# Kernel optimization log

Measured on AMD Instinct MI355X. Metric: run time of the kernel, lower is better.

The kernel has to match this reference:

```python
import jax, jax.numpy as jnp
import numpy as np
from jax import lax

MAX_U = 5
MAX_V = 5
BN_EPS = 1e-5


def _conv(x, w, b, p):
    # NCHW conv with symmetric padding p (torch Conv2d padding=p)
    y = lax.conv_general_dilated(x, w, (1, 1), [(p, p), (p, p)],
                                 dimension_numbers=('NCHW', 'OIHW', 'NCHW'))
    return y + b[None, :, None, None]


def _branch(x, w3, b3, w5, b5, w7, b7):
    a3 = jax.nn.relu(_conv(x, w3, b3, 1))
    a5 = jax.nn.relu(_conv(jnp.concatenate([a3, x], 1), w5, b5, 2))
    a7 = jax.nn.relu(_conv(jnp.concatenate([a5, x], 1), w7, b7, 3))
    return jnp.concatenate([a3, a5, a7], 1)  # [B, 448, H, W]


def _dct_basis(n, kmax, dtype):
    # orthonormal DCT-II basis rows for frequencies u < kmax: [kmax, n]
    i = jnp.arange(n, dtype=dtype)
    u = jnp.arange(kmax, dtype=dtype)
    basis = jnp.cos(jnp.pi * (2.0 * i[None, :] + 1.0) * u[:, None] / (2.0 * n))
    scale = jnp.where(u == 0, jnp.sqrt(1.0 / n), jnp.sqrt(2.0 / n))
    return basis * scale[:, None]


def setup_inputs() -> dict:
    key = jax.random.key(0)
    ks = iter(jax.random.split(key, 64))

    def w(shape, s=0.05):
        return (jax.random.normal(next(ks), shape, jnp.float32) * s)

    cin = 3  # input_channels per group (x has 2*cin = 6 channels)
    inp = {"x": jax.random.normal(next(ks), (16, 6, 64, 64), jnp.float32)}
    for g in (1, 2):
        for b in (1, 2):
            inp[f"g{g}b{b}c3_w"] = w((64, cin, 3, 3))
            inp[f"g{g}b{b}c3_b"] = w((64,))
            inp[f"g{g}b{b}c5_w"] = w((128, 64 + cin, 5, 5))
            inp[f"g{g}b{b}c5_b"] = w((128,))
            inp[f"g{g}b{b}c7_w"] = w((256, 128 + cin, 7, 7))
            inp[f"g{g}b{b}c7_b"] = w((256,))
    inp["gap_w"] = w((12, 1792)); inp["gap_b"] = w((12,))
    inp["dct_w"] = w((12, 1792)); inp["dct_b"] = w((12,))
    inp["bn_gamma"] = jnp.ones((1792,), jnp.float32)
    inp["bn_beta"] = jnp.zeros((1792,), jnp.float32)
    inp["bn_mean"] = jnp.zeros((1792,), jnp.float32)
    inp["bn_var"] = jnp.ones((1792,), jnp.float32)
    return inp


def reference(x,
              g1b1c3_w, g1b1c3_b, g1b1c5_w, g1b1c5_b, g1b1c7_w, g1b1c7_b,
              g1b2c3_w, g1b2c3_b, g1b2c5_w, g1b2c5_b, g1b2c7_w, g1b2c7_b,
              g2b1c3_w, g2b1c3_b, g2b1c5_w, g2b1c5_b, g2b1c7_w, g2b1c7_b,
              g2b2c3_w, g2b2c3_b, g2b2c5_w, g2b2c5_b, g2b2c7_w, g2b2c7_b,
              gap_w, gap_b, dct_w, dct_b, bn_gamma, bn_beta, bn_mean, bn_var):
    B, C, H, W = x.shape  # C is even (6)
    half = C // 2
    x1, x2 = x[:, :half], x[:, half:]
    out1 = jnp.concatenate([
        _branch(x1, g1b1c3_w, g1b1c3_b, g1b1c5_w, g1b1c5_b, g1b1c7_w, g1b1c7_b),
        _branch(x1, g1b2c3_w, g1b2c3_b, g1b2c5_w, g1b2c5_b, g1b2c7_w, g1b2c7_b)], 1)
    out2 = jnp.concatenate([
        _branch(x2, g2b1c3_w, g2b1c3_b, g2b1c5_w, g2b1c5_b, g2b1c7_w, g2b1c7_b),
        _branch(x2, g2b2c3_w, g2b2c3_b, g2b2c5_w, g2b2c5_b, g2b2c7_w, g2b2c7_b)], 1)
    concat_out = jnp.concatenate([out1, out2], 1)  # [B, 1792, H, W]

    # GAP head
    gap = concat_out.mean((2, 3))  # [B, 1792]
    gap_pred = gap @ gap_w.T + gap_b

    # Batched multi-frequency DCT compression: low-frequency 5x5 block of the
    # 2D DCT-II of each channel, averaged -> one scalar per channel.
    Bh = _dct_basis(H, MAX_U, x.dtype)  # [5, H]
    Bw = _dct_basis(W, MAX_V, x.dtype)  # [5, W]
    coeff = jnp.einsum('bchw,uh,vw->bcuv', concat_out, Bh, Bw)  # [B,1792,5,5]
    dct_feat = coeff.mean((2, 3))  # [B, 1792]

    # BatchNorm1d (inference with running stats); dropout is identity in eval.
    bn = bn_gamma * (dct_feat - bn_mean) / jnp.sqrt(bn_var + BN_EPS) + bn_beta
    dct_pred = bn @ dct_w.T + dct_b
    return gap_pred, dct_pred
```

## Files before the change

kernel.cpp:

```cpp
#include <hip/hip_runtime.h>
#include <hip/hip_bf16.h>
#include <math.h>

#define HW 64
#define NPIX 4096
#define NB 16
#define NCH 1792

typedef __bf16 bf16;
typedef __bf16 bf16x8 __attribute__((ext_vector_type(8)));
typedef float f32x4 __attribute__((ext_vector_type(4)));

struct PtrQuad { const float* p[4]; };

constexpr size_t W3SZ = 9 * 1 * 64 * 32;
constexpr size_t W5SZ = 25 * 3 * 128 * 32;
constexpr size_t W7SZ = 49 * 5 * 256 * 32;
constexpr size_t WBR  = W3SZ + W5SZ + W7SZ;

__global__ __launch_bounds__(256) void init_kernel(float* __restrict__ gap_sum,
                                                   float* __restrict__ dct_sum,
                                                   float* __restrict__ dctw) {
    int tid = blockIdx.x * 256 + threadIdx.x;
    if (tid < NB * NCH) { gap_sum[tid] = 0.f; dct_sum[tid] = 0.f; }
    if (blockIdx.x == 0 && threadIdx.x < HW) {
        int i = threadIdx.x;
        float s = 0.f;
        for (int u = 0; u < 5; ++u) {
            float scale = (u == 0) ? 0.125f : 0.17677669529663687f;
            s += cosf(3.14159265358979323846f * (2.f * i + 1.f) * u / 128.f) * scale;
        }
        dctw[i] = s * 0.2f;
    }
}

__global__ __launch_bounds__(256) void prep_x_kernel(const float* __restrict__ x,
                                                     bf16* __restrict__ xpad) {
    int tid = blockIdx.x * 256 + threadIdx.x;
    if (tid >= NB * 2 * NPIX * 32) return;
    int c = tid & 31;
    int pix = (tid >> 5) & (NPIX - 1);
    int g = (tid >> 17) & 1;
    int b = tid >> 18;
    float v = (c < 3) ? x[((size_t)(b * 6 + g * 3 + c)) * NPIX + pix] : 0.f;
    xpad[tid] = (bf16)v;
}

template <int K, int CHUNKS, int CIN_ACT, int COUT>
__global__ __launch_bounds__(256) void prep_w_all(PtrQuad src, bf16* __restrict__ dst) {
    constexpr int CIN = CIN_ACT + 3;
    constexpr int TOT = K * K * CHUNKS * COUT * 32;
    int tid = blockIdx.x * 256 + threadIdx.x;
    if (tid >= 4 * TOT) return;
    int br = tid / TOT;
    int idx = tid - br * TOT;
    int cc = idx & 31;
    int co = (idx >> 5) % COUT;
    int rest = idx / (32 * COUT);
    int chunk = rest % CHUNKS;
    int ks = rest / CHUNKS;
    int ky = ks / K, kx = ks % K;
    int ci;
    if (chunk < CHUNKS - 1) ci = chunk * 32 + cc;
    else ci = (cc < 3) ? (CIN_ACT + cc) : -1;
    const float* w = src.p[br];
    float v = (ci >= 0) ? w[(((size_t)co * CIN + ci) * K + ky) * K + kx] : 0.f;
    dst[(size_t)br * WBR + idx] = (bf16)v;
}

template <int K, int CHUNKS, int COUT, int NBLK, bool STORE>
__global__ __launch_bounds__(256, 2) void conv_mfma(
    const bf16* __restrict__ act_in, size_t a_in_brs,
    const bf16* __restrict__ xpad,
    const bf16* __restrict__ wall, size_t stage_woff,
    PtrQuad biasq,
    bf16* __restrict__ act_out, size_t a_out_brs,
    float* __restrict__ gap_sum, float* __restrict__ dct_sum,
    int stage_coff, const float* __restrict__ dctw, int br0)
{
    constexpr int PAD = K / 2;
    constexpr int R = 4;
    constexpr int HR = R + K - 1;
    constexpr int WC = HW + K - 1;
    constexpr int ACT_CHUNKS = CHUNKS - 1;
    constexpr int AS = ACT_CHUNKS * 32;
    constexpr int WN = NBLK / 32;
    constexpr int NUNITS = 4 * HR * WC;
    constexpr int SEGU = HR * WC + 1;
    constexpr int CW = CHUNKS * COUT * 32;

    __shared__ __align__(16) bf16 s_in[4 * SEGU * 8];

    const int tid = threadIdx.x;
    const int lane = tid & 63;
    const int wv = tid >> 6;
    const int wm = wv >> 1;
    const int wn = wv & 1;
    const int q = lane >> 4;
    const int ln = lane & 15;

    const int bz = blockIdx.z;
    const int b = bz & 15;
    const int lbr = bz >> 4;
    const int br = br0 + lbr;
    const int g = br >> 1;

    const int row0 = blockIdx.x * R;
    const int n0g = blockIdx.y * NBLK + wn * (NBLK / 2);

    const bf16* wrep = wall + (size_t)br * WBR + stage_woff;
    const float* bias = biasq.p[br];

    int abase[8];
#pragma unroll
    for (int t = 0; t < 8; ++t) {
        int lr = wm * 2 + (t >> 2);
        int ct = (t & 3) * 16;
        abase[t] = (q * SEGU + lr * WC + ct + ln) * 8;
    }
    const int lane_w = ln * 32 + q * 8;

    f32x4 acc[8][WN];
#pragma unroll
    for (int t = 0; t < 8; ++t)
#pragma unroll
        for (int u = 0; u < WN; ++u) acc[t][u] = f32x4{0.f, 0.f, 0.f, 0.f};

    const bf16* xsrc = xpad + ((size_t)(b * 2 + g)) * NPIX * 32;
    const bf16* actb = act_in + lbr * a_in_brs + (size_t)b * NPIX * AS;

#pragma unroll 1
    for (int chunk = 0; chunk < CHUNKS; ++chunk) {
        __syncthreads();
        const bf16* src;
        int stride;
        if (chunk < ACT_CHUNKS) { src = actb + chunk * 32; stride = AS; }
        else                    { src = xsrc;              stride = 32; }
        for (int uidx = tid; uidx < NUNITS; uidx += 256) {
            int kseg = uidx / (HR * WC);
            int rem = uidx - kseg * (HR * WC);
            int rr = rem / WC;
            int col = rem - rr * WC;
            int gr = row0 + rr - PAD;
            int gc = col - PAD;
            bf16x8 v;
#pragma unroll
            for (int j = 0; j < 8; ++j) v[j] = (bf16)0.f;
            if (gr >= 0 && gr < HW && gc >= 0 && gc < HW)
                v = *(const bf16x8*)(src + (size_t)(gr * HW + gc) * stride + kseg * 8);
            *(bf16x8*)(s_in + (kseg * SEGU + rem) * 8) = v;
        }
        __syncthreads();

        const bf16* wchunk = wrep + ((size_t)chunk * COUT + n0g) * 32 + lane_w;

#pragma unroll 1
        for (int ky = 0; ky < K; ++ky) {
            const bf16* wky = wchunk + (size_t)(ky * K) * CW;
            const int kyoff = ky * WC * 8;
#pragma unroll
            for (int kx = 0; kx < K; ++kx) {
                const int koff = kyoff + kx * 8;
                const bf16* wstep = wky + (size_t)kx * CW;
                bf16x8 bfr[WN];
#pragma unroll
                for (int u = 0; u < WN; ++u)
                    bfr[u] = *(const bf16x8*)(wstep + u * 512);
                bf16x8 afr[8];
#pragma unroll
                for (int t = 0; t < 8; ++t)
                    afr[t] = *(const bf16x8*)(s_in + abase[t] + koff);
#pragma unroll
                for (int t = 0; t < 8; ++t)
#pragma unroll
                    for (int u = 0; u < WN; ++u)
                        acc[t][u] = __builtin_amdgcn_mfma_f32_16x16x32_bf16(
                            afr[t], bfr[u], acc[t][u], 0, 0, 0);
            }
        }
    }

    float gsum[WN], dsum[WN], bv[WN];
#pragma unroll
    for (int u = 0; u < WN; ++u) {
        gsum[u] = 0.f; dsum[u] = 0.f;
        bv[u] = bias[n0g + u * 16 + ln];
    }

    bf16* outb = act_out + lbr * a_out_brs;

#pragma unroll
    for (int t = 0; t < 8; ++t) {
        const int lr = wm * 2 + (t >> 2);
        const int gr = row0 + lr;
        const float wrow = dctw[gr];
        const int ct = (t & 3) * 16;
#pragma unroll
        for (int r = 0; r < 4; ++r) {
            const int gc = ct + q * 4 + r;
            const float wcd = dctw[gc] * wrow;
            const size_t pixoff = ((size_t)b * NPIX + gr * HW + gc) * COUT;
#pragma unroll
            for (int u = 0; u < WN; ++u) {
                float v = fmaxf(acc[t][u][r] + bv[u], 0.f);
                if constexpr (STORE)
                    outb[pixoff + n0g + u * 16 + ln] = (bf16)v;
                gsum[u] += v;
                dsum[u] = fmaf(v, wcd, dsum[u]);
            }
        }
    }

    const int chan_base = br * 448 + stage_coff;
#pragma unroll
    for (int u = 0; u < WN; ++u) {
        float gv = gsum[u], dv = dsum[u];
        gv += __shfl_xor(gv, 16, 64); gv += __shfl_xor(gv, 32, 64);
        dv += __shfl_xor(dv, 16, 64); dv += __shfl_xor(dv, 32, 64);
        if (q == 0) {
            int ch = chan_base + n0g + u * 16 + ln;
            atomicAdd(&gap_sum[b * NCH + ch], gv);
            atomicAdd(&dct_sum[b * NCH + ch], dv);
        }
    }
}

__global__ __launch_bounds__(256) void head_kernel(
    const float* __restrict__ gap_sum, const float* __restrict__ dct_sum,
    const float* __restrict__ gap_w, const float* __restrict__ gap_b,
    const float* __restrict__ dct_w, const float* __restrict__ dct_b,
    const float* __restrict__ gamma, const float* __restrict__ beta,
    const float* __restrict__ mean, const float* __restrict__ var,
    float* __restrict__ out)
{
    const int blk = blockIdx.x;
    const int b = blk / 24;
    const int rem = blk - b * 24;
    const int kind = rem / 12;
    const int i = rem - kind * 12;
    const int tid = threadIdx.x;

    float partial = 0.f;
    if (kind == 0) {
        for (int cc = tid; cc < NCH; cc += 256)
            partial += gap_sum[b * NCH + cc] * (1.f / 4096.f) * gap_w[i * NCH + cc];
    } else {
        for (int cc = tid; cc < NCH; cc += 256) {
            float f = dct_sum[b * NCH + cc];
            f = gamma[cc] * (f - mean[cc]) * rsqrtf(var[cc] + 1e-5f) + beta[cc];
            partial += f * dct_w[i * NCH + cc];
        }
    }
#pragma unroll
    for (int off = 32; off > 0; off >>= 1) partial += __shfl_down(partial, off, 64);
    __shared__ float red[4];
    if ((tid & 63) == 0) red[tid >> 6] = partial;
    __syncthreads();
    if (tid == 0) {
        float tot = red[0] + red[1] + red[2] + red[3];
        tot += (kind == 0 ? gap_b[i] : dct_b[i]);
        out[kind * (NB * 12) + b * 12 + i] = tot;
    }
}

extern "C" void kernel_launch(void* const* d_in, const int* in_sizes, int n_in,
                              void* d_out, int out_size, void* d_ws, size_t ws_size,
                              hipStream_t stream)
{
    const float* x = (const float*)d_in[0];

    float* fws = (float*)d_ws;
    float* dctw    = fws;
    float* gap_sum = fws + 64;
    float* dct_sum = gap_sum + NB * NCH;
    bf16* bws = (bf16*)(dct_sum + NB * NCH);

    const size_t XPSZ = (size_t)NB * 2 * NPIX * 32;
    const size_t A3B  = (size_t)NB * NPIX * 64;
    const size_t A5B  = (size_t)NB * NPIX * 128;

    const size_t fixed = 229632 + 2 * (XPSZ + 4 * WBR);
    int nbr = 1;
    if (ws_size >= fixed + 2 * 4 * (A3B + A5B)) nbr = 4;
    else if (ws_size >= fixed + 2 * 2 * (A3B + A5B)) nbr = 2;

    bf16* xpad = bws;
    bf16* wall = xpad + XPSZ;
    bf16* a3   = wall + 4 * WBR;
    bf16* a5   = a3 + (size_t)nbr * A3B;

    hipLaunchKernelGGL(init_kernel, dim3((NB * NCH + 255) / 256), dim3(256), 0, stream,
                       gap_sum, dct_sum, dctw);
    hipLaunchKernelGGL(prep_x_kernel, dim3((NB * 2 * NPIX * 32) / 256), dim3(256), 0, stream,
                       x, xpad);

    PtrQuad w3q = {{(const float*)d_in[1], (const float*)d_in[7], (const float*)d_in[13], (const float*)d_in[19]}};
    PtrQuad b3q = {{(const float*)d_in[2], (const float*)d_in[8], (const float*)d_in[14], (const float*)d_in[20]}};
    PtrQuad w5q = {{(const float*)d_in[3], (const float*)d_in[9], (const float*)d_in[15], (const float*)d_in[21]}};
    PtrQuad b5q = {{(const float*)d_in[4], (const float*)d_in[10], (const float*)d_in[16], (const float*)d_in[22]}};
    PtrQuad w7q = {{(const float*)d_in[5], (const float*)d_in[11], (const float*)d_in[17], (const float*)d_in[23]}};
    PtrQuad b7q = {{(const float*)d_in[6], (const float*)d_in[12], (const float*)d_in[18], (const float*)d_in[24]}};

    hipLaunchKernelGGL((prep_w_all<3, 1, 0, 64>), dim3((4 * W3SZ + 255) / 256), dim3(256), 0, stream,
                       w3q, wall);
    hipLaunchKernelGGL((prep_w_all<5, 3, 64, 128>), dim3((4 * W5SZ + 255) / 256), dim3(256), 0, stream,
                       w5q, wall + W3SZ);
    hipLaunchKernelGGL((prep_w_all<7, 5, 128, 256>), dim3((4 * W7SZ + 255) / 256), dim3(256), 0, stream,
                       w7q, wall + W3SZ + W5SZ);

    for (int br0 = 0; br0 < 4; br0 += nbr) {
        hipLaunchKernelGGL((conv_mfma<3, 1, 64, 64, true>), dim3(16, 1, NB * nbr), dim3(256), 0, stream,
                           (const bf16*)nullptr, 0, xpad, wall, 0, b3q,
                           a3, A3B, gap_sum, dct_sum, 0, dctw, br0);
        hipLaunchKernelGGL((conv_mfma<5, 3, 128, 128, true>), dim3(16, 1, NB * nbr), dim3(256), 0, stream,
                           a3, A3B, xpad, wall, W3SZ, b5q,
                           a5, A5B, gap_sum, dct_sum, 64, dctw, br0);
        hipLaunchKernelGGL((conv_mfma<7, 5, 256, 128, false>), dim3(16, 2, NB * nbr), dim3(256), 0, stream,
                           a5, A5B, xpad, wall, W3SZ + W5SZ, b7q,
                           (bf16*)nullptr, 0, gap_sum, dct_sum, 192, dctw, br0);
    }

    hipLaunchKernelGGL(head_kernel, dim3(NB * 24), dim3(256), 0, stream,
                       gap_sum, dct_sum,
                       (const float*)d_in[25], (const float*)d_in[26],
                       (const float*)d_in[27], (const float*)d_in[28],
                       (const float*)d_in[29], (const float*)d_in[30],
                       (const float*)d_in[31], (const float*)d_in[32],
                       (float*)d_out);
}
```

Before: 1.002 ms.

## Pre-pad activations into planar layout and double-buffer chunks via global_load_lds

Activations and input are stored as zero-padded 72-wide planes of 8 channels, so tile loads no longer need bounds checks. Input tiles are copied straight into LDS with async global_load_lds into two buffers, so loading the next chunk overlaps the MFMA work on the current one. Blocks grow to 512 threads covering 8 rows. A zeroing pass over the larger padded buffers adds memory traffic. LDS use doubles and the 512-thread, 2-block launch bound limits registers per thread, which may cause spills.

```diff
diff --git a/kernel.cpp b/kernel.cpp
--- a/kernel.cpp
+++ b/kernel.cpp
@@ -6,6 +6,9 @@
 #define NPIX 4096
 #define NB 16
 #define NCH 1792
+#define PW 72
+#define PROWS 70
+#define PLANE (PROWS * PW)
 
 typedef __bf16 bf16;
 typedef __bf16 bf16x8 __attribute__((ext_vector_type(8)));
@@ -17,6 +20,7 @@
 constexpr size_t W5SZ = 25 * 3 * 128 * 32;
 constexpr size_t W7SZ = 49 * 5 * 256 * 32;
 constexpr size_t WBR  = W3SZ + W5SZ + W7SZ;
+constexpr size_t PLE  = (size_t)PLANE * 8;
 
 __global__ __launch_bounds__(256) void init_kernel(float* __restrict__ gap_sum,
                                                    float* __restrict__ dct_sum,
@@ -34,16 +38,23 @@
     }
 }
 
+__global__ __launch_bounds__(256) void zero_kernel(float4* __restrict__ p, long n) {
+    long i = (long)blockIdx.x * 256 + threadIdx.x;
+    long stride = (long)gridDim.x * 256;
+    for (; i < n; i += stride) p[i] = float4{0.f, 0.f, 0.f, 0.f};
+}
+
 __global__ __launch_bounds__(256) void prep_x_kernel(const float* __restrict__ x,
-                                                     bf16* __restrict__ xpad) {
+                                                     bf16* __restrict__ xp) {
     int tid = blockIdx.x * 256 + threadIdx.x;
-    if (tid >= NB * 2 * NPIX * 32) return;
-    int c = tid & 31;
-    int pix = (tid >> 5) & (NPIX - 1);
-    int g = (tid >> 17) & 1;
-    int b = tid >> 18;
-    float v = (c < 3) ? x[((size_t)(b * 6 + g * 3 + c)) * NPIX + pix] : 0.f;
-    xpad[tid] = (bf16)v;
+    if (tid >= NB * 2 * NPIX) return;
+    int pix = tid & (NPIX - 1);
+    int g = (tid >> 12) & 1;
+    int b = tid >> 13;
+    int h = pix >> 6, w = pix & 63;
+    size_t base = ((size_t)(b * 2 + g) * 4) * PLE + ((size_t)(h + 3) * PW + (w + 3)) * 8;
+    for (int c = 0; c < 3; ++c)
+        xp[base + c] = (bf16)x[((size_t)(b * 6 + g * 3 + c)) * NPIX + pix];
 }
 
 template <int K, int CHUNKS, int CIN_ACT, int COUT>
@@ -69,35 +80,38 @@
 }
 
 template <int K, int CHUNKS, int COUT, int NBLK, bool STORE>
-__global__ __launch_bounds__(256, 2) void conv_mfma(
-    const bf16* __restrict__ act_in, size_t a_in_brs,
+__global__ __launch_bounds__(512, 2) void conv_mfma(
+    const bf16* __restrict__ act_in,
     const bf16* __restrict__ xpad,
     const bf16* __restrict__ wall, size_t stage_woff,
     PtrQuad biasq,
-    bf16* __restrict__ act_out, size_t a_out_brs,
+    bf16* __restrict__ act_out,
     float* __restrict__ gap_sum, float* __restrict__ dct_sum,
     int stage_coff, const float* __restrict__ dctw, int br0)
 {
     constexpr int PAD = K / 2;
-    constexpr int R = 4;
-    constexpr int HR = R + K - 1;
-    constexpr int WC = HW + K - 1;
+    constexpr int COFF = 3 - PAD;
+    constexpr int HR = 8 + K - 1;
+    constexpr int RH = HR / 2;
+    constexpr int UN = RH * PW;
+    constexpr int NI = (UN + 63) / 64;
+    constexpr int BUFU = 4 * HR * PW;
     constexpr int ACT_CHUNKS = CHUNKS - 1;
-    constexpr int AS = ACT_CHUNKS * 32;
     constexpr int WN = NBLK / 32;
-    constexpr int NUNITS = 4 * HR * WC;
-    constexpr int SEGU = HR * WC + 1;
     constexpr int CW = CHUNKS * COUT * 32;
-
-    __shared__ __align__(16) bf16 s_in[4 * SEGU * 8];
+    constexpr int OPL = COUT / 8;
+
+    __shared__ __align__(16) bf16 s_in[2 * BUFU * 8];
 
     const int tid = threadIdx.x;
     const int lane = tid & 63;
     const int wv = tid >> 6;
-    const int wm = wv >> 1;
+    const int wavem = wv >> 1;
     const int wn = wv & 1;
     const int q = lane >> 4;
     const int ln = lane & 15;
+    const int sseg = wv >> 1;
+    const int shalf = wv & 1;
 
     const int bz = blockIdx.z;
     const int b = bz & 15;
@@ -105,20 +119,21 @@
     const int br = br0 + lbr;
     const int g = br >> 1;
 
-    const int row0 = blockIdx.x * R;
-    const int n0g = blockIdx.y * NBLK + wn * (NBLK / 2);
+    const int o0 = blockIdx.x * 8;
+    const int prow0 = o0 + COFF;
+    const int n0 = blockIdx.y * NBLK + wn * (NBLK / 2);
 
     const bf16* wrep = wall + (size_t)br * WBR + stage_woff;
     const float* bias = biasq.p[br];
+    const size_t img = (size_t)(lbr * NB + b);
 
     int abase[8];
 #pragma unroll
     for (int t = 0; t < 8; ++t) {
-        int lr = wm * 2 + (t >> 2);
+        int lr = wavem * 2 + (t >> 2);
         int ct = (t & 3) * 16;
-        abase[t] = (q * SEGU + lr * WC + ct + ln) * 8;
-    }
-    const int lane_w = ln * 32 + q * 8;
+        abase[t] = ((q * HR + lr) * PW + ct + ln + COFF) * 8;
+    }
 
     f32x4 acc[8][WN];
 #pragma unroll
@@ -126,50 +141,44 @@
 #pragma unroll
         for (int u = 0; u < WN; ++u) acc[t][u] = f32x4{0.f, 0.f, 0.f, 0.f};
 
-    const bf16* xsrc = xpad + ((size_t)(b * 2 + g)) * NPIX * 32;
-    const bf16* actb = act_in + lbr * a_in_brs + (size_t)b * NPIX * AS;
-
-#pragma unroll 1
-    for (int chunk = 0; chunk < CHUNKS; ++chunk) {
-        __syncthreads();
-        const bf16* src;
-        int stride;
-        if (chunk < ACT_CHUNKS) { src = actb + chunk * 32; stride = AS; }
-        else                    { src = xsrc;              stride = 32; }
-        for (int uidx = tid; uidx < NUNITS; uidx += 256) {
-            int kseg = uidx / (HR * WC);
-            int rem = uidx - kseg * (HR * WC);
-            int rr = rem / WC;
-            int col = rem - rr * WC;
-            int gr = row0 + rr - PAD;
-            int gc = col - PAD;
-            bf16x8 v;
-#pragma unroll
-            for (int j = 0; j < 8; ++j) v[j] = (bf16)0.f;
-            if (gr >= 0 && gr < HW && gc >= 0 && gc < HW)
-                v = *(const bf16x8*)(src + (size_t)(gr * HW + gc) * stride + kseg * 8);
-            *(bf16x8*)(s_in + (kseg * SEGU + rem) * 8) = v;
-        }
-        __syncthreads();
-
-        const bf16* wchunk = wrep + ((size_t)chunk * COUT + n0g) * 32 + lane_w;
-
+    auto issue = [&](int chunk, int sel) {
+        const bf16* pl;
+        if (chunk < ACT_CHUNKS)
+            pl = act_in + (img * (ACT_CHUNKS * 4) + chunk * 4 + sseg) * PLE;
+        else
+            pl = xpad + ((size_t)((b * 2 + g) * 4 + sseg)) * PLE;
+        const bf16* gb = pl + (size_t)(prow0 + shalf * RH) * PW * 8;
+        const bf16* lb = s_in + ((size_t)sel * BUFU + (sseg * HR + shalf * RH) * PW) * 8;
+#pragma unroll
+        for (int i = 0; i < NI; ++i) {
+            int u = i * 64 + lane;
+            if (u < UN)
+                __builtin_amdgcn_global_load_lds(
+                    (const __attribute__((address_space(1))) void*)(gb + (size_t)u * 8),
+                    (__attribute__((address_space(3))) void*)(lb + i * 512),
+                    16, 0, 0);
+        }
+    };
+
+    auto compute = [&](int chunk, int sel) {
+        const bf16* buf = s_in + (size_t)sel * BUFU * 8;
+        const bf16* wchunk = wrep + ((size_t)chunk * COUT + n0) * 32 + ln * 32 + q * 8;
 #pragma unroll 1
         for (int ky = 0; ky < K; ++ky) {
             const bf16* wky = wchunk + (size_t)(ky * K) * CW;
-            const int kyoff = ky * WC * 8;
+            const int kyoff = ky * PW * 8;
 #pragma unroll
             for (int kx = 0; kx < K; ++kx) {
-                const int koff = kyoff + kx * 8;
                 const bf16* wstep = wky + (size_t)kx * CW;
                 bf16x8 bfr[WN];
 #pragma unroll
                 for (int u = 0; u < WN; ++u)
                     bfr[u] = *(const bf16x8*)(wstep + u * 512);
+                const int koff = kyoff + kx * 8;
                 bf16x8 afr[8];
 #pragma unroll
                 for (int t = 0; t < 8; ++t)
-                    afr[t] = *(const bf16x8*)(s_in + abase[t] + koff);
+                    afr[t] = *(const bf16x8*)(buf + abase[t] + koff);
 #pragma unroll
                 for (int t = 0; t < 8; ++t)
 #pragma unroll
@@ -178,47 +187,60 @@
                             afr[t], bfr[u], acc[t][u], 0, 0, 0);
             }
         }
-    }
+    };
+
+    issue(0, 0);
+#pragma unroll 1
+    for (int c = 0; c < CHUNKS - 1; ++c) {
+        issue(c + 1, (c + 1) & 1);
+        __builtin_amdgcn_s_waitcnt(0xF70 | NI);
+        __builtin_amdgcn_s_barrier();
+        compute(c, c & 1);
+        __builtin_amdgcn_s_barrier();
+    }
+    __builtin_amdgcn_s_waitcnt(0xF70);
+    __builtin_amdgcn_s_barrier();
+    compute(CHUNKS - 1, (CHUNKS - 1) & 1);
 
     float gsum[WN], dsum[WN], bv[WN];
 #pragma unroll
     for (int u = 0; u < WN; ++u) {
         gsum[u] = 0.f; dsum[u] = 0.f;
-        bv[u] = bias[n0g + u * 16 + ln];
-    }
-
-    bf16* outb = act_out + lbr * a_out_brs;
+        bv[u] = bias[n0 + u * 16 + ln];
+    }
 
 #pragma unroll
     for (int t = 0; t < 8; ++t) {
-        const int lr = wm * 2 + (t >> 2);
-        const int gr = row0 + lr;
+        const int lr = wavem * 2 + (t >> 2);
+        const int gr = o0 + lr;
         const float wrow = dctw[gr];
         const int ct = (t & 3) * 16;
 #pragma unroll
         for (int r = 0; r < 4; ++r) {
             const int gc = ct + q * 4 + r;
             const float wcd = dctw[gc] * wrow;
-            const size_t pixoff = ((size_t)b * NPIX + gr * HW + gc) * COUT;
 #pragma unroll
             for (int u = 0; u < WN; ++u) {
                 float v = fmaxf(acc[t][u][r] + bv[u], 0.f);
-                if constexpr (STORE)
-                    outb[pixoff + n0g + u * 16 + ln] = (bf16)v;
+                if constexpr (STORE) {
+                    int ch = n0 + u * 16 + ln;
+                    act_out[(img * OPL + (ch >> 3)) * PLE +
+                            ((size_t)(gr + 3) * PW + (gc + 3)) * 8 + (ch & 7)] = (bf16)v;
+                }
                 gsum[u] += v;
                 dsum[u] = fmaf(v, wcd, dsum[u]);
             }
         }
     }
 
-    const int chan_base = br * 448 + stage_coff;
+    const int cb = br * 448 + stage_coff;
 #pragma unroll
     for (int u = 0; u < WN; ++u) {
         float gv = gsum[u], dv = dsum[u];
         gv += __shfl_xor(gv, 16, 64); gv += __shfl_xor(gv, 32, 64);
         dv += __shfl_xor(dv, 16, 64); dv += __shfl_xor(dv, 32, 64);
         if (q == 0) {
-            int ch = chan_base + n0g + u * 16 + ln;
+            int ch = cb + n0 + u * 16 + ln;
             atomicAdd(&gap_sum[b * NCH + ch], gv);
             atomicAdd(&dct_sum[b * NCH + ch], dv);
         }
@@ -275,24 +297,28 @@
     float* dct_sum = gap_sum + NB * NCH;
     bf16* bws = (bf16*)(dct_sum + NB * NCH);
 
-    const size_t XPSZ = (size_t)NB * 2 * NPIX * 32;
-    const size_t A3B  = (size_t)NB * NPIX * 64;
-    const size_t A5B  = (size_t)NB * NPIX * 128;
-
-    const size_t fixed = 229632 + 2 * (XPSZ + 4 * WBR);
+    const size_t WALL_E = 4 * WBR;
+    const size_t XP_E   = (size_t)NB * 2 * 4 * PLE;
+    const size_t A3_BR  = (size_t)NB * 8 * PLE;
+    const size_t A5_BR  = (size_t)NB * 16 * PLE;
+
+    const size_t fixed_b = 229632 + 2 * (WALL_E + XP_E);
     int nbr = 1;
-    if (ws_size >= fixed + 2 * 4 * (A3B + A5B)) nbr = 4;
-    else if (ws_size >= fixed + 2 * 2 * (A3B + A5B)) nbr = 2;
-
-    bf16* xpad = bws;
-    bf16* wall = xpad + XPSZ;
-    bf16* a3   = wall + 4 * WBR;
-    bf16* a5   = a3 + (size_t)nbr * A3B;
+    if (ws_size >= fixed_b + 2 * 4 * (A3_BR + A5_BR)) nbr = 4;
+    else if (ws_size >= fixed_b + 2 * 2 * (A3_BR + A5_BR)) nbr = 2;
+
+    bf16* wall = bws;
+    bf16* xp   = wall + WALL_E;
+    bf16* a3p  = xp + XP_E;
+    bf16* a5p  = a3p + (size_t)nbr * A3_BR;
 
     hipLaunchKernelGGL(init_kernel, dim3((NB * NCH + 255) / 256), dim3(256), 0, stream,
                        gap_sum, dct_sum, dctw);
-    hipLaunchKernelGGL(prep_x_kernel, dim3((NB * 2 * NPIX * 32) / 256), dim3(256), 0, stream,
-                       x, xpad);
+
+    const long zero16 = (long)((XP_E + (size_t)nbr * (A3_BR + A5_BR)) * 2 / 16);
+    hipLaunchKernelGGL(zero_kernel, dim3(2048), dim3(256), 0, stream, (float4*)xp, zero16);
+
+    hipLaunchKernelGGL(prep_x_kernel, dim3((NB * 2 * NPIX) / 256), dim3(256), 0, stream, x, xp);
 
     PtrQuad w3q = {{(const float*)d_in[1], (const float*)d_in[7], (const float*)d_in[13], (const float*)d_in[19]}};
     PtrQuad b3q = {{(const float*)d_in[2], (const float*)d_in[8], (const float*)d_in[14], (const float*)d_in[20]}};
@@ -301,23 +327,20 @@
     PtrQuad w7q = {{(const float*)d_in[5], (const float*)d_in[11], (const float*)d_in[17], (const float*)d_in[23]}};
     PtrQuad b7q = {{(const float*)d_in[6], (const float*)d_in[12], (const float*)d_in[18], (const float*)d_in[24]}};
 
-    hipLaunchKernelGGL((prep_w_all<3, 1, 0, 64>), dim3((4 * W3SZ + 255) / 256), dim3(256), 0, stream,
-                       w3q, wall);
-    hipLaunchKernelGGL((prep_w_all<5, 3, 64, 128>), dim3((4 * W5SZ + 255) / 256), dim3(256), 0, stream,
-                       w5q, wall + W3SZ);
-    hipLaunchKernelGGL((prep_w_all<7, 5, 128, 256>), dim3((4 * W7SZ + 255) / 256), dim3(256), 0, stream,
-                       w7q, wall + W3SZ + W5SZ);
+    hipLaunchKernelGGL((prep_w_all<3, 1, 0, 64>), dim3((4 * W3SZ + 255) / 256), dim3(256), 0, stream, w3q, wall);
+    hipLaunchKernelGGL((prep_w_all<5, 3, 64, 128>), dim3((4 * W5SZ + 255) / 256), dim3(256), 0, stream, w5q, wall + W3SZ);
+    hipLaunchKernelGGL((prep_w_all<7, 5, 128, 256>), dim3((4 * W7SZ + 255) / 256), dim3(256), 0, stream, w7q, wall + W3SZ + W5SZ);
 
     for (int br0 = 0; br0 < 4; br0 += nbr) {
-        hipLaunchKernelGGL((conv_mfma<3, 1, 64, 64, true>), dim3(16, 1, NB * nbr), dim3(256), 0, stream,
-                           (const bf16*)nullptr, 0, xpad, wall, 0, b3q,
-                           a3, A3B, gap_sum, dct_sum, 0, dctw, br0);
-        hipLaunchKernelGGL((conv_mfma<5, 3, 128, 128, true>), dim3(16, 1, NB * nbr), dim3(256), 0, stream,
-                           a3, A3B, xpad, wall, W3SZ, b5q,
-                           a5, A5B, gap_sum, dct_sum, 64, dctw, br0);
-        hipLaunchKernelGGL((conv_mfma<7, 5, 256, 128, false>), dim3(16, 2, NB * nbr), dim3(256), 0, stream,
-                           a5, A5B, xpad, wall, W3SZ + W5SZ, b7q,
-                           (bf16*)nullptr, 0, gap_sum, dct_sum, 192, dctw, br0);
+        hipLaunchKernelGGL((conv_mfma<3, 1, 64, 64, true>), dim3(8, 1, NB * nbr), dim3(512), 0, stream,
+                           (const bf16*)nullptr, xp, wall, 0, b3q,
+                           a3p, gap_sum, dct_sum, 0, dctw, br0);
+        hipLaunchKernelGGL((conv_mfma<5, 3, 128, 128, true>), dim3(8, 1, NB * nbr), dim3(512), 0, stream,
+                           a3p, xp, wall, W3SZ, b5q,
+                           a5p, gap_sum, dct_sum, 64, dctw, br0);
+        hipLaunchKernelGGL((conv_mfma<7, 5, 256, 128, false>), dim3(8, 2, NB * nbr), dim3(512), 0, stream,
+                           a5p, xp, wall, W3SZ + W5SZ, b7q,
+                           (bf16*)nullptr, gap_sum, dct_sum, 192, dctw, br0);
     }
 
     hipLaunchKernelGGL(head_kernel, dim3(NB * 24), dim3(256), 0, stream,
```

New measurement: 1.014 ms. Within noise of the previous version (+1.2%).
